# Kernel tuning notes

Measured on AMD Instinct MI355X. Metric: run time of the kernel, lower is better.

## Reference

```python
import math
import jax, jax.numpy as jnp
import numpy as np

S, E = 8192, 64
CAPACITY_FACTOR = 1.0
MIN_CAPACITY = 2


def setup_inputs() -> dict:
    key = jax.random.key(0)
    k1, k2 = jax.random.split(key)
    logits = jax.random.normal(k1, (S, E), dtype=jnp.float32)
    noise = jax.random.normal(k2, (S, E), dtype=jnp.float32)
    return {"logits": logits, "noise": noise}


def reference(logits, noise):
    s, e = logits.shape
    # _capacity: ceil(tokens/experts * capacity_factor*2), min-clamped; static under jit
    capacity = int(max(MIN_CAPACITY, math.ceil((s / e) * CAPACITY_FACTOR * 2.0)))

    gates = jax.nn.softmax(logits, axis=1)                      # [s,e]
    idx1 = jnp.argmax(gates, axis=1)                            # [s]
    mask1 = jax.nn.one_hot(idx1, e, dtype=jnp.int32)            # [s,e]

    neg_min = jnp.finfo(logits.dtype).min
    logits_w_noise = logits + noise
    logits_except1 = jnp.where(mask1.astype(bool), neg_min, logits_w_noise)
    idx2 = jnp.argmax(logits_except1, axis=1)
    mask2 = jax.nn.one_hot(idx2, e, dtype=jnp.int32)            # [s,e]

    locations1 = jnp.cumsum(mask1, axis=0) - 1                  # [s,e]
    locations2 = jnp.cumsum(mask2, axis=0) - 1 + jnp.sum(mask1, axis=0, keepdims=True)

    me = jnp.mean(gates, axis=0)                                # [e]
    ce = jnp.mean(mask1.astype(logits.dtype), axis=0)           # [e]
    l_aux = jnp.mean(me * ce * e * e)

    # drop tokens over capacity
    mask1 = mask1 * (locations1 < capacity).astype(jnp.int32)
    mask2 = mask2 * (locations2 < capacity).astype(jnp.int32)

    locations1_s = jnp.sum(locations1 * mask1, axis=1)          # [s]
    locations2_s = jnp.sum(locations2 * mask2, axis=1)          # [s]
    locations1_sc = jax.nn.one_hot(locations1_s, capacity, dtype=logits.dtype)  # [s,c]
    locations2_sc = jax.nn.one_hot(locations2_s, capacity, dtype=logits.dtype)

    mask1_f = mask1.astype(logits.dtype)
    mask2_f = mask2.astype(logits.dtype)
    gates1_s = jnp.sum(gates * mask1_f, axis=1)                 # [s]
    gates2_s = jnp.sum(gates * mask2_f, axis=1)
    denom_s = jnp.maximum(gates1_s + gates2_s, jnp.finfo(logits.dtype).eps)
    gates1_s = gates1_s / denom_s
    gates2_s = gates2_s / denom_s

    combine_weights = (
        jnp.einsum('s,se,sc->sec', gates1_s, mask1_f, locations1_sc)
        + jnp.einsum('s,se,sc->sec', gates2_s, mask2_f, locations2_sc)
    )  # [s,e,c]
    dispatch_mask = combine_weights.astype(bool)
    return (l_aux, combine_weights, dispatch_mask)
```

## Files before the change

kernel.cpp:

```cpp
#include <hip/hip_runtime.h>


namespace {
constexpr int  TOK  = 8192;
constexpr int  NEXP = 64;
constexpr int  CAPC = 256;
constexpr int  CHK  = 128;
constexpr int  NCHK = TOK / CHK;
constexpr long long TBLK = (long long)NEXP * CAPC;
constexpr long long SEC  = (long long)TOK * TBLK;
constexpr float NEGMIN = -3.402823466e38f;
constexpr float EPSF   = 1.1920929e-7f;
constexpr long long PK_OFF  = 16380LL * 16384 + 8;
constexpr long long H12_OFF = 16380LL * 16384 + 8200;
constexpr long long G1_OFF  = 16381LL * 16384 + 8;
constexpr long long ME_OFF  = 16381LL * 16384 + 8200;
constexpr long long G2_OFF  = 16382LL * 16384 + 8;
constexpr long long B12_OFF = 16382LL * 16384 + 8200;
}

typedef float f32x4 __attribute__((ext_vector_type(4)));

__device__ __forceinline__ float wave_max64(float v) {
    for (int o = 32; o; o >>= 1) v = fmaxf(v, __shfl_xor(v, o));
    return v;
}
__device__ __forceinline__ float wave_sum64(float v) {
    for (int o = 32; o; o >>= 1) v += __shfl_xor(v, o);
    return v;
}

__global__ __launch_bounds__(1024) void tg_gate(const float* __restrict__ logits,
                                                const float* __restrict__ noise,
                                                float* __restrict__ out)
{
    __shared__ int   i12s[CHK];
    __shared__ float g1s[CHK], g2s[CHK];
    __shared__ int   cntA[2][NEXP];
    __shared__ int   cntB[2][NEXP];
    __shared__ int   lrS[2][2][64];
    __shared__ float meSh[1024];
    const int tid = threadIdx.x, lane = tid & 63, wv = tid >> 6;
    const int c = blockIdx.x;

    float meAcc = 0.f;
    #pragma unroll
    for (int i = 0; i < CHK / 16; ++i) {
        const int rloc = i * 16 + wv;
        const int row  = c * CHK + rloc;
        const float l = logits[row * NEXP + lane];
        const float n = noise [row * NEXP + lane];

        const float m    = wave_max64(l);
        const float ex   = __expf(l - m);
        const float sm   = wave_sum64(ex);
        const float gate = ex / sm;

        const unsigned long long b1 = __ballot(l == m);
        const int   i1 = __ffsll(b1) - 1;
        const float G1 = __shfl(gate, i1);

        const float lw = (lane == i1) ? NEGMIN : (l + n);
        const float m2 = wave_max64(lw);
        const unsigned long long b2 = __ballot(lw == m2);
        const int   i2 = __ffsll(b2) - 1;
        const float G2 = __shfl(gate, i2);

        if (lane == 0) {
            i12s[rloc] = i1 | (i2 << 8);
            g1s[rloc]  = G1;
            g2s[rloc]  = G2;
        }
        meAcc += gate;
    }
    meSh[tid] = meAcc;
    if      (tid < 128) cntA[tid >> 6][tid & 63] = 0;
    else if (tid < 256) cntB[(tid - 128) >> 6][tid & 63] = 0;
    __syncthreads();

    if (wv < 4) {
        const int half = wv & 1;
        const int sel  = wv >> 1;
        const int t    = half * 64 + lane;
        const int pk   = i12s[t];
        const int e    = sel ? ((pk >> 8) & 255) : (pk & 255);
        unsigned long long m = ~0ull;
        #pragma unroll
        for (int b = 0; b < 6; ++b) {
            const unsigned long long bb = __ballot((e >> b) & 1);
            m &= ((e >> b) & 1) ? bb : ~bb;
        }
        const unsigned long long below = (1ull << lane) - 1;
        lrS[sel][half][lane] = __popcll(m & below);
        if ((m & below) == 0) {
            (half ? cntB : cntA)[sel][e] = __popcll(m);
        }
    }
    __syncthreads();

    int* outi = (int*)out;
    if (tid < 128) {
        const int t = tid, pk = i12s[t];
        const int h = t >> 6, ln = t & 63;
        const int e1 = pk & 255, e2 = (pk >> 8) & 255;
        const int r1 = lrS[0][h][ln] + (h ? cntA[0][e1] : 0);
        const int r2 = lrS[1][h][ln] + (h ? cntA[1][e2] : 0);
        outi[PK_OFF + c * CHK + t] = (pk & 0xffff) | (r1 << 16) | (r2 << 24);
        out [G1_OFF + c * CHK + t] = g1s[t];
        out [G2_OFF + c * CHK + t] = g2s[t];
    }
    if (tid < NEXP) {
        const int h1 = cntA[0][tid] + cntB[0][tid];
        const int h2 = cntA[1][tid] + cntB[1][tid];
        outi[H12_OFF + c * NEXP + tid] = h1 | (h2 << 16);
        float s = 0.f;
        #pragma unroll
        for (int w = 0; w < 16; ++w) s += meSh[w * 64 + tid];
        out[ME_OFF + c * NEXP + tid] = s;
    }
}

__global__ __launch_bounds__(256) void tg_scan(float* __restrict__ out)
{
    __shared__ int   h1s[NCHK][NEXP];
    __shared__ int   h2s[NCHK][NEXP];
    __shared__ float mes[NCHK][NEXP];
    const int tid = threadIdx.x;
    const int* outi = (const int*)out;
    for (int n = tid; n < NCHK * NEXP; n += 256) {
        const int v = outi[H12_OFF + n];
        h1s[n >> 6][n & 63] = v & 0xffff;
        h2s[n >> 6][n & 63] = v >> 16;
        mes[n >> 6][n & 63] = out[ME_OFF + n];
    }
    __syncthreads();
    if (tid < NEXP) {
        const int e = tid;
        int r1 = 0, r2 = 0;
        float ms = 0.f;
        for (int c = 0; c < NCHK; ++c) {
            const int h = h1s[c][e];
            h1s[c][e] = r1;
            r1 += h; r2 += h2s[c][e]; ms += mes[c][e];
        }
        int p2 = r1;
        int* wbi = (int*)out;
        for (int c = 0; c < NCHK; ++c) {
            wbi[B12_OFF + c * NEXP + e] = h1s[c][e] | (p2 << 16);
            p2 += h2s[c][e];
        }
        float term = (ms * (1.f / TOK)) * ((float)r1 * (1.f / TOK)) * (float)(NEXP * NEXP);
        term = wave_sum64(term);
        if (e == 0) out[0] = term * (1.f / NEXP);
    }
}

__global__ __launch_bounds__(256) void tg_emit(float* __restrict__ out)
{
    const int s = blockIdx.x * 256 + threadIdx.x;
    const int c = s >> 7;
    const int* outi = (const int*)out;
    const int   pk = outi[PK_OFF + s];
    const float G1 = out[G1_OFF + s];
    const float G2 = out[G2_OFF + s];
    const int i1 = pk & 255, i2 = (pk >> 8) & 255;
    const unsigned b1w = (unsigned)outi[B12_OFF + c * NEXP + i1];
    const unsigned b2w = (unsigned)outi[B12_OFF + c * NEXP + i2];
    const int loc1 = (int)(b1w & 0xffffu) + ((pk >> 16) & 255);
    const int loc2 = (int)(b2w >> 16)     + ((pk >> 24) & 255);

    const bool k1 = loc1 < CAPC, k2 = loc2 < CAPC;
    const float ge1 = k1 ? G1 : 0.f, ge2 = k2 ? G2 : 0.f;
    const float dn  = fmaxf(ge1 + ge2, EPSF);
    const float w1 = ge1 / dn, w2 = ge2 / dn;
    const int rec0 = i1 | (i2 << 8) | (k1 ? 1 << 16 : 0) | (k2 ? 1 << 17 : 0);
    const int rec1 = (k1 ? loc1 : 0) | ((k2 ? loc2 : 0) << 16);
    const int j1 = k1 ? (i1 * CAPC + (rec1 & 0xffff) + 1) : -1;
    const int j2 = k2 ? (i2 * CAPC + (rec1 >> 16) + 1) : -1;

    long long h = (long long)s * TBLK;
    ((int*)out)[h + 1] = rec0;
    ((int*)out)[h + 2] = rec1;
    out[h + 3] = w1;
    out[h + 4] = w2;
    out[h + TBLK] = (j1 == (int)TBLK) ? w1 : ((j2 == (int)TBLK) ? w2 : 0.f);

    h = (long long)(TOK + s) * TBLK;
    ((int*)out)[h + 1] = rec0;
    ((int*)out)[h + 2] = rec1;
    out[h + 3] = 1.f;
    out[h + 4] = 1.f;
    out[h + TBLK] = (j1 == (int)TBLK || j2 == (int)TBLK) ? 1.f : 0.f;
}

__global__ __launch_bounds__(256) void tg_write(float* __restrict__ out)
{
    const int lane = threadIdx.x & 63, wv = threadIdx.x >> 6;
    const int w = blockIdx.x * 4 + wv;
    float* base = out + (long long)w * TBLK;

    const f32x4 A  = *(const f32x4*)base;
    const float v2 = base[4];

    const float sv  = A.x;
    const int  rec0 = __float_as_int(A.y);
    const int  rec1 = __float_as_int(A.z);
    const float v1  = A.w;
    const bool k1 = (rec0 >> 16) & 1, k2 = (rec0 >> 17) & 1;
    const int  i1 = rec0 & 255, i2 = (rec0 >> 8) & 255;
    const int  j1 = k1 ? (i1 * CAPC + (rec1 & 0xffff) + 1) : -1;
    const int  j2 = k2 ? (i2 * CAPC + (rec1 >> 16) + 1) : -1;

    f32x4* b4 = (f32x4*)base;
    #pragma unroll
    for (int i = 0; i < 64; ++i) {
        const int q = i * 64 + lane;
        const int j = q * 4;
        f32x4 v;
        v.x = (j     == j1) ? v1 : ((j     == j2) ? v2 : 0.f);
        v.y = (j + 1 == j1) ? v1 : ((j + 1 == j2) ? v2 : 0.f);
        v.z = (j + 2 == j1) ? v1 : ((j + 2 == j2) ? v2 : 0.f);
        v.w = (j + 3 == j1) ? v1 : ((j + 3 == j2) ? v2 : 0.f);
        if (q == 0) v.x = sv;
        __builtin_nontemporal_store(v, &b4[q]);
    }
}

extern "C" void kernel_launch(void* const* d_in, const int* in_sizes, int n_in,
                              void* d_out, int out_size, void* d_ws, size_t ws_size,
                              hipStream_t stream)
{
    (void)d_ws; (void)ws_size; (void)in_sizes; (void)n_in; (void)out_size;
    const float* logits = (const float*)d_in[0];
    const float* noise  = (const float*)d_in[1];
    float* out = (float*)d_out;

    tg_gate <<<NCHK,      1024, 0, stream>>>(logits, noise, out);
    tg_scan <<<1,          256, 0, stream>>>(out);
    tg_emit <<<TOK / 256,  256, 0, stream>>>(out);
    tg_write<<<TOK / 2,    256, 0, stream>>>(out);
}
```

Measured before the change: 213.2 us.

## Halve gate chunk size, simplify scan, and write zeros then scatter nonzeros

```diff
diff --git a/kernel.cpp b/kernel.cpp
--- a/kernel.cpp
+++ b/kernel.cpp
@@ -5,18 +5,18 @@
 constexpr int  TOK  = 8192;
 constexpr int  NEXP = 64;
 constexpr int  CAPC = 256;
-constexpr int  CHK  = 128;
+constexpr int  CHK  = 64;
 constexpr int  NCHK = TOK / CHK;
 constexpr long long TBLK = (long long)NEXP * CAPC;
 constexpr long long SEC  = (long long)TOK * TBLK;
 constexpr float NEGMIN = -3.402823466e38f;
 constexpr float EPSF   = 1.1920929e-7f;
-constexpr long long PK_OFF  = 16380LL * 16384 + 8;
-constexpr long long H12_OFF = 16380LL * 16384 + 8200;
-constexpr long long G1_OFF  = 16381LL * 16384 + 8;
-constexpr long long ME_OFF  = 16381LL * 16384 + 8200;
-constexpr long long G2_OFF  = 16382LL * 16384 + 8;
-constexpr long long B12_OFF = 16382LL * 16384 + 8200;
+constexpr long long PK_OFF  = 16377LL * TBLK + 8;
+constexpr long long G1_OFF  = 16378LL * TBLK + 8;
+constexpr long long G2_OFF  = 16379LL * TBLK + 8;
+constexpr long long H12_OFF = 16380LL * TBLK + 8;
+constexpr long long ME_OFF  = 16381LL * TBLK + 8;
+constexpr long long B12_OFF = 16382LL * TBLK + 8;
 }
 
 typedef float f32x4 __attribute__((ext_vector_type(4)));
@@ -30,23 +30,24 @@
     return v;
 }
 
-__global__ __launch_bounds__(1024) void tg_gate(const float* __restrict__ logits,
-                                                const float* __restrict__ noise,
-                                                float* __restrict__ out)
+__global__ __launch_bounds__(512) void tg_gate(const float* __restrict__ logits,
+                                               const float* __restrict__ noise,
+                                               float* __restrict__ out)
 {
     __shared__ int   i12s[CHK];
     __shared__ float g1s[CHK], g2s[CHK];
-    __shared__ int   cntA[2][NEXP];
-    __shared__ int   cntB[2][NEXP];
-    __shared__ int   lrS[2][2][64];
-    __shared__ float meSh[1024];
+    __shared__ int   lr1s[CHK], lr2s[CHK];
+    __shared__ int   cnt[2][NEXP];
+    __shared__ float meSh[512];
     const int tid = threadIdx.x, lane = tid & 63, wv = tid >> 6;
     const int c = blockIdx.x;
 
+    if (tid < 128) cnt[tid >> 6][tid & 63] = 0;
+
     float meAcc = 0.f;
     #pragma unroll
-    for (int i = 0; i < CHK / 16; ++i) {
-        const int rloc = i * 16 + wv;
+    for (int i = 0; i < CHK / 8; ++i) {
+        const int rloc = i * 8 + wv;
         const int row  = c * CHK + rloc;
         const float l = logits[row * NEXP + lane];
         const float n = noise [row * NEXP + lane];
@@ -74,16 +75,12 @@
         meAcc += gate;
     }
     meSh[tid] = meAcc;
-    if      (tid < 128) cntA[tid >> 6][tid & 63] = 0;
-    else if (tid < 256) cntB[(tid - 128) >> 6][tid & 63] = 0;
     __syncthreads();
 
-    if (wv < 4) {
-        const int half = wv & 1;
-        const int sel  = wv >> 1;
-        const int t    = half * 64 + lane;
-        const int pk   = i12s[t];
-        const int e    = sel ? ((pk >> 8) & 255) : (pk & 255);
+    if (wv < 2) {
+        const int sel = wv;
+        const int pk  = i12s[lane];
+        const int e   = sel ? ((pk >> 8) & 255) : (pk & 255);
         unsigned long long m = ~0ull;
         #pragma unroll
         for (int b = 0; b < 6; ++b) {
@@ -91,74 +88,57 @@
             m &= ((e >> b) & 1) ? bb : ~bb;
         }
         const unsigned long long below = (1ull << lane) - 1;
-        lrS[sel][half][lane] = __popcll(m & below);
-        if ((m & below) == 0) {
-            (half ? cntB : cntA)[sel][e] = __popcll(m);
-        }
+        (sel ? lr2s : lr1s)[lane] = __popcll(m & below);
+        if ((m & below) == 0) cnt[sel][e] = __popcll(m);
     }
     __syncthreads();
 
     int* outi = (int*)out;
-    if (tid < 128) {
-        const int t = tid, pk = i12s[t];
-        const int h = t >> 6, ln = t & 63;
-        const int e1 = pk & 255, e2 = (pk >> 8) & 255;
-        const int r1 = lrS[0][h][ln] + (h ? cntA[0][e1] : 0);
-        const int r2 = lrS[1][h][ln] + (h ? cntA[1][e2] : 0);
-        outi[PK_OFF + c * CHK + t] = (pk & 0xffff) | (r1 << 16) | (r2 << 24);
-        out [G1_OFF + c * CHK + t] = g1s[t];
-        out [G2_OFF + c * CHK + t] = g2s[t];
+    if (tid < CHK) {
+        const int pk = i12s[tid];
+        outi[PK_OFF + c * CHK + tid] = (pk & 0xffff) | (lr1s[tid] << 16) | (lr2s[tid] << 24);
+        out [G1_OFF + c * CHK + tid] = g1s[tid];
+        out [G2_OFF + c * CHK + tid] = g2s[tid];
     }
     if (tid < NEXP) {
-        const int h1 = cntA[0][tid] + cntB[0][tid];
-        const int h2 = cntA[1][tid] + cntB[1][tid];
-        outi[H12_OFF + c * NEXP + tid] = h1 | (h2 << 16);
+        outi[H12_OFF + c * NEXP + tid] = cnt[0][tid] | (cnt[1][tid] << 16);
         float s = 0.f;
         #pragma unroll
-        for (int w = 0; w < 16; ++w) s += meSh[w * 64 + tid];
+        for (int w = 0; w < 8; ++w) s += meSh[w * 64 + tid];
         out[ME_OFF + c * NEXP + tid] = s;
     }
 }
 
-__global__ __launch_bounds__(256) void tg_scan(float* __restrict__ out)
-{
-    __shared__ int   h1s[NCHK][NEXP];
-    __shared__ int   h2s[NCHK][NEXP];
-    __shared__ float mes[NCHK][NEXP];
-    const int tid = threadIdx.x;
+__global__ __launch_bounds__(64) void tg_scan(float* __restrict__ out)
+{
+    const int e = threadIdx.x;
     const int* outi = (const int*)out;
-    for (int n = tid; n < NCHK * NEXP; n += 256) {
-        const int v = outi[H12_OFF + n];
-        h1s[n >> 6][n & 63] = v & 0xffff;
-        h2s[n >> 6][n & 63] = v >> 16;
-        mes[n >> 6][n & 63] = out[ME_OFF + n];
-    }
-    __syncthreads();
-    if (tid < NEXP) {
-        const int e = tid;
-        int r1 = 0, r2 = 0;
-        float ms = 0.f;
-        for (int c = 0; c < NCHK; ++c) {
-            const int h = h1s[c][e];
-            h1s[c][e] = r1;
-            r1 += h; r2 += h2s[c][e]; ms += mes[c][e];
-        }
-        int p2 = r1;
-        int* wbi = (int*)out;
-        for (int c = 0; c < NCHK; ++c) {
-            wbi[B12_OFF + c * NEXP + e] = h1s[c][e] | (p2 << 16);
-            p2 += h2s[c][e];
-        }
-        float term = (ms * (1.f / TOK)) * ((float)r1 * (1.f / TOK)) * (float)(NEXP * NEXP);
-        term = wave_sum64(term);
-        if (e == 0) out[0] = term * (1.f / NEXP);
-    }
+    int* wbi = (int*)out;
+
+    int t1 = 0, t2 = 0;
+    float ms = 0.f;
+    for (int c = 0; c < NCHK; ++c) {
+        const int h = outi[H12_OFF + c * NEXP + e];
+        t1 += h & 0xffff;
+        t2 += h >> 16;
+        ms += out[ME_OFF + c * NEXP + e];
+    }
+    int p1 = 0, p2 = t1;
+    for (int c = 0; c < NCHK; ++c) {
+        const int h = outi[H12_OFF + c * NEXP + e];
+        wbi[B12_OFF + c * NEXP + e] = p1 | (p2 << 16);
+        p1 += h & 0xffff;
+        p2 += h >> 16;
+    }
+    float term = (ms * (1.f / TOK)) * ((float)t1 * (1.f / TOK)) * (float)(NEXP * NEXP);
+    term = wave_sum64(term);
+    if (e == 0) out[0] = term * (1.f / NEXP);
 }
 
 __global__ __launch_bounds__(256) void tg_emit(float* __restrict__ out)
 {
     const int s = blockIdx.x * 256 + threadIdx.x;
-    const int c = s >> 7;
+    const int c = s >> 6;
     const int* outi = (const int*)out;
     const int   pk = outi[PK_OFF + s];
     const float G1 = out[G1_OFF + s];
@@ -201,28 +181,26 @@
 
     const f32x4 A  = *(const f32x4*)base;
     const float v2 = base[4];
-
     const float sv  = A.x;
     const int  rec0 = __float_as_int(A.y);
     const int  rec1 = __float_as_int(A.z);
     const float v1  = A.w;
     const bool k1 = (rec0 >> 16) & 1, k2 = (rec0 >> 17) & 1;
     const int  i1 = rec0 & 255, i2 = (rec0 >> 8) & 255;
-    const int  j1 = k1 ? (i1 * CAPC + (rec1 & 0xffff) + 1) : -1;
-    const int  j2 = k2 ? (i2 * CAPC + (rec1 >> 16) + 1) : -1;
+    const int  j1 = i1 * CAPC + (rec1 & 0xffff) + 1;
+    const int  j2 = i2 * CAPC + (rec1 >> 16) + 1;
 
     f32x4* b4 = (f32x4*)base;
+    const f32x4 z = {0.f, 0.f, 0.f, 0.f};
     #pragma unroll
-    for (int i = 0; i < 64; ++i) {
-        const int q = i * 64 + lane;
-        const int j = q * 4;
-        f32x4 v;
-        v.x = (j     == j1) ? v1 : ((j     == j2) ? v2 : 0.f);
-        v.y = (j + 1 == j1) ? v1 : ((j + 1 == j2) ? v2 : 0.f);
-        v.z = (j + 2 == j1) ? v1 : ((j + 2 == j2) ? v2 : 0.f);
-        v.w = (j + 3 == j1) ? v1 : ((j + 3 == j2) ? v2 : 0.f);
-        if (q == 0) v.x = sv;
-        __builtin_nontemporal_store(v, &b4[q]);
+    for (int i = 0; i < 64; ++i)
+        __builtin_nontemporal_store(z, &b4[i * 64 + lane]);
+
+    asm volatile("s_waitcnt vmcnt(0)" ::: "memory");
+    if (lane == 0) {
+        base[0] = sv;
+        if (k1) base[j1] = v1;
+        if (k2) base[j2] = v2;
     }
 }
 
@@ -235,8 +213,8 @@
     const float* noise  = (const float*)d_in[1];
     float* out = (float*)d_out;
 
-    tg_gate <<<NCHK,      1024, 0, stream>>>(logits, noise, out);
-    tg_scan <<<1,          256, 0, stream>>>(out);
-    tg_emit <<<TOK / 256,  256, 0, stream>>>(out);
-    tg_write<<<TOK / 2,    256, 0, stream>>>(out);
-}
+    tg_gate <<<NCHK,      512, 0, stream>>>(logits, noise, out);
+    tg_scan <<<1,          64, 0, stream>>>(out);
+    tg_emit <<<TOK / 256, 256, 0, stream>>>(out);
+    tg_write<<<TOK / 2,   256, 0, stream>>>(out);
+}
```

New measurement: 216.6 us. About the same (+1.6%).
